# Kernel optimization log

Measured on AMD Instinct MI355X. Metric: run time of the kernel, lower is better.

Reference implementation:

```python
import jax, jax.numpy as jnp
import numpy as np

K = 3          # k_neighbors
EPS = 1e-12    # F.normalize eps


def _l2norm(x):
    n = jnp.sqrt(jnp.sum(x * x, axis=-1, keepdims=True))
    return x / jnp.maximum(n, EPS)


def setup_inputs() -> dict:
    key = jax.random.key(0)
    k1, k2 = jax.random.split(key)
    query_features = jax.random.normal(k1, (64, 64, 32, 32), dtype=jnp.float32)
    support_features = jax.random.normal(k2, (64, 5, 64, 1024), dtype=jnp.float32)
    return {"query_features": query_features, "support_features": support_features}


def reference(query_features, support_features):
    B, D, h, w = query_features.shape
    # (B, Nq, D), L2-normalized along D
    q_local = _l2norm(query_features.reshape(B, D, h * w).transpose(0, 2, 1))
    # support: (B, Way, D, Ns) -> (B, Way, Ns, D), L2-normalized along D
    s_local = _l2norm(support_features.transpose(0, 1, 3, 2))
    # cosine similarities for all (batch, way) pairs in one batched matmul
    sim = jnp.einsum('bqd,bwsd->bwqs', q_local, s_local)  # (B, Way, Nq, Ns)
    k_actual = min(K, sim.shape[-1])
    topk_sim, _ = jax.lax.top_k(sim, k_actual)            # (B, Way, Nq, k)
    return topk_sim.sum(axis=(-1, -2))                    # (B, Way)
```

## Files before the change

### kernel.cpp

```cpp
#include <hip/hip_runtime.h>
#include <hip/hip_bf16.h>


using bf16x8 = __attribute__((ext_vector_type(8))) short;
using f32x4  = __attribute__((ext_vector_type(4))) float;

__device__ inline unsigned short f2bf(float f) {
    unsigned int u = __float_as_uint(f);
    u += 0x7fffu + ((u >> 16) & 1u);
    return (unsigned short)(u >> 16);
}

__device__ inline uint4 pack8(const float* v) {
    uint4 r;
    r.x = (unsigned)f2bf(v[0]) | ((unsigned)f2bf(v[1]) << 16);
    r.y = (unsigned)f2bf(v[2]) | ((unsigned)f2bf(v[3]) << 16);
    r.z = (unsigned)f2bf(v[4]) | ((unsigned)f2bf(v[5]) << 16);
    r.w = (unsigned)f2bf(v[6]) | ((unsigned)f2bf(v[7]) << 16);
    return r;
}

#define INS(v, T0, T1, T2) do {                         \
    float _v = (v);                                     \
    float _n0 = fmaxf((T0), _v);                        \
    float _n1 = __builtin_amdgcn_fmed3f(_v, (T0), (T1));\
    float _n2 = __builtin_amdgcn_fmed3f(_v, (T1), (T2));\
    (T0) = _n0; (T1) = _n1; (T2) = _n2;                 \
} while (0)

__global__ void norms_kernel(const float* __restrict__ Q, const float* __restrict__ S,
                             float* __restrict__ rnq, float* __restrict__ rns) {
    int gid = blockIdx.x * blockDim.x + threadIdx.x;
    if (gid < 65536) {
        int b = gid >> 10, qi = gid & 1023;
        const float* p = Q + (size_t)b * 65536 + qi;
        float ss = 0.f;
        #pragma unroll
        for (int d = 0; d < 64; ++d) { float v = p[(size_t)d * 1024]; ss += v * v; }
        rnq[gid] = 1.0f / fmaxf(sqrtf(ss), 1e-12f);
    } else {
        int v = gid - 65536;
        int bw = v >> 10, si = v & 1023;
        const float* p = S + (size_t)bw * 65536 + si;
        float ss = 0.f;
        #pragma unroll
        for (int d = 0; d < 64; ++d) { float x = p[(size_t)d * 1024]; ss += x * x; }
        rns[v] = 1.0f / fmaxf(sqrtf(ss), 1e-12f);
    }
}

__global__ __launch_bounds__(512) void knn_main(
        const float* __restrict__ Q, const float* __restrict__ S,
        const float* __restrict__ rnq, const float* __restrict__ rns,
        float* __restrict__ partial) {
    __shared__ uint4 qfrag[16 * 128];
    __shared__ uint4 sfrag[2][4 * 128];
    __shared__ float wsum[8];

    const int qc = blockIdx.x, w = blockIdx.y, b = blockIdx.z;
    const int t = threadIdx.x, wv = t >> 6, lane = t & 63;

    const float* Qb   = Q + (size_t)b * 65536;
    const float* Sb   = S + (size_t)(b * 5 + w) * 65536;
    const float* rnqb = rnq + (b << 10);
    const float* rnsb = rns + ((b * 5 + w) << 10);

    for (int sub = 0; sub < 4; ++sub) {
        int qg = (qc << 8) + (sub << 6) + lane;
        float r = rnqb[qg];
        float v[8];
        #pragma unroll
        for (int i = 0; i < 8; ++i)
            v[i] = Qb[(size_t)((wv << 3) + i) * 1024 + qg] * r;
        qfrag[((sub << 2) + (lane >> 4)) * 128 + (wv << 4) + (lane & 15)] = pack8(v);
    }
    __syncthreads();

    bf16x8 bq[2][2];
    #pragma unroll
    for (int qt = 0; qt < 2; ++qt)
        #pragma unroll
        for (int c = 0; c < 2; ++c)
            bq[qt][c] = *reinterpret_cast<const bf16x8*>(
                &qfrag[((wv << 1) + qt) * 128 + (c << 6) + lane]);

    {
        float sv[8]; float rs = rnsb[lane];
        #pragma unroll
        for (int i = 0; i < 8; ++i)
            sv[i] = Sb[(size_t)((wv << 3) + i) * 1024 + lane] * rs;
        sfrag[0][(lane >> 4) * 128 + (wv << 4) + (lane & 15)] = pack8(sv);
    }
    __syncthreads();

    float t0[2] = {-1e30f, -1e30f}, t1[2] = {-1e30f, -1e30f}, t2[2] = {-1e30f, -1e30f};
    int cur = 0;

    for (int blk = 0; blk < 16; ++blk) {
        float sv[8];
        if (blk < 15) {
            const int sb = (blk + 1) << 6;
            float rs = rnsb[sb + lane];
            #pragma unroll
            for (int i = 0; i < 8; ++i)
                sv[i] = Sb[(size_t)((wv << 3) + i) * 1024 + sb + lane] * rs;
        }
        #pragma unroll
        for (int st = 0; st < 4; ++st) {
            bf16x8 a0 = *reinterpret_cast<const bf16x8*>(&sfrag[cur][st * 128 + lane]);
            bf16x8 a1 = *reinterpret_cast<const bf16x8*>(&sfrag[cur][st * 128 + 64 + lane]);
            #pragma unroll
            for (int qt = 0; qt < 2; ++qt) {
                f32x4 c = {0.f, 0.f, 0.f, 0.f};
                c = __builtin_amdgcn_mfma_f32_16x16x32_bf16(a0, bq[qt][0], c, 0, 0, 0);
                c = __builtin_amdgcn_mfma_f32_16x16x32_bf16(a1, bq[qt][1], c, 0, 0, 0);
                #pragma unroll
                for (int j = 0; j < 4; ++j)
                    INS(c[j], t0[qt], t1[qt], t2[qt]);
            }
        }
        if (blk < 15)
            sfrag[cur ^ 1][(lane >> 4) * 128 + (wv << 4) + (lane & 15)] = pack8(sv);
        __syncthreads();
        cur ^= 1;
    }

    #pragma unroll
    for (int qt = 0; qt < 2; ++qt) {
        #pragma unroll
        for (int m = 16; m <= 32; m <<= 1) {
            float b0 = __shfl_xor(t0[qt], m);
            float b1 = __shfl_xor(t1[qt], m);
            float b2 = __shfl_xor(t2[qt], m);
            INS(b0, t0[qt], t1[qt], t2[qt]);
            INS(b1, t0[qt], t1[qt], t2[qt]);
            INS(b2, t0[qt], t1[qt], t2[qt]);
        }
    }
    float s3 = (t0[0] + t1[0] + t2[0]) + (t0[1] + t1[1] + t2[1]);
    #pragma unroll
    for (int m = 1; m < 64; m <<= 1) s3 += __shfl_xor(s3, m);
    s3 *= 0.25f;
    if (lane == 0) wsum[wv] = s3;
    __syncthreads();
    if (t == 0) {
        float acc = 0.f;
        #pragma unroll
        for (int i = 0; i < 8; ++i) acc += wsum[i];
        partial[((size_t)(b * 5 + w) << 2) + qc] = acc;
    }
}

__global__ void finalize_kernel(const float* __restrict__ partial, float* __restrict__ out) {
    int i = blockIdx.x * blockDim.x + threadIdx.x;
    if (i < 320)
        out[i] = (partial[4 * i] + partial[4 * i + 1]) +
                 (partial[4 * i + 2] + partial[4 * i + 3]);
}

extern "C" void kernel_launch(void* const* d_in, const int* in_sizes, int n_in,
                              void* d_out, int out_size, void* d_ws, size_t ws_size,
                              hipStream_t stream) {
    const float* Q = (const float*)d_in[0];
    const float* S = (const float*)d_in[1];
    float* out = (float*)d_out;

    float* rnq = (float*)d_ws;
    float* rns = rnq + 65536;
    float* partial = rns + 327680;

    norms_kernel<<<(65536 + 327680) / 256, 256, 0, stream>>>(Q, S, rnq, rns);
    dim3 grid(4, 5, 64);
    knn_main<<<grid, 512, 0, stream>>>(Q, S, rnq, rns, partial);
    finalize_kernel<<<2, 256, 0, stream>>>(partial, out);
}
```

Before: 108.6 us.

## Double queries per block, defer query normalization, use hardware bf16 pack

Each block now covers 512 queries instead of 256, loading them in two phases through the same shared buffer. Each wave holds four query tiles, so every staged support tile is reused across twice as many MFMAs, and the grid shrinks to half the blocks. Query normalization moves to after top-k: the raw dot products are ranked and the selected sum is scaled by the query's inverse norm, which is valid because that norm is positive and the same for all of a query's candidates. The software bf16 rounding is replaced with the v_cvt_pk_bf16_f32 instruction, and the launch bounds gain an occupancy hint. Risks include higher register pressure from the extra accumulators and fragments, and fewer blocks to fill the GPU.

```diff
diff --git a/kernel.cpp b/kernel.cpp
--- a/kernel.cpp
+++ b/kernel.cpp
@@ -5,18 +5,18 @@
 using bf16x8 = __attribute__((ext_vector_type(8))) short;
 using f32x4  = __attribute__((ext_vector_type(4))) float;
 
-__device__ inline unsigned short f2bf(float f) {
-    unsigned int u = __float_as_uint(f);
-    u += 0x7fffu + ((u >> 16) & 1u);
-    return (unsigned short)(u >> 16);
+__device__ inline unsigned cvt_pk_bf16(float lo, float hi) {
+    unsigned r;
+    asm("v_cvt_pk_bf16_f32 %0, %1, %2" : "=v"(r) : "v"(lo), "v"(hi));
+    return r;
 }
 
-__device__ inline uint4 pack8(const float* v) {
+__device__ inline uint4 pack8cvt(const float* v) {
     uint4 r;
-    r.x = (unsigned)f2bf(v[0]) | ((unsigned)f2bf(v[1]) << 16);
-    r.y = (unsigned)f2bf(v[2]) | ((unsigned)f2bf(v[3]) << 16);
-    r.z = (unsigned)f2bf(v[4]) | ((unsigned)f2bf(v[5]) << 16);
-    r.w = (unsigned)f2bf(v[6]) | ((unsigned)f2bf(v[7]) << 16);
+    r.x = cvt_pk_bf16(v[0], v[1]);
+    r.y = cvt_pk_bf16(v[2], v[3]);
+    r.z = cvt_pk_bf16(v[4], v[5]);
+    r.w = cvt_pk_bf16(v[6], v[7]);
     return r;
 }
 
@@ -49,7 +49,7 @@
     }
 }
 
-__global__ __launch_bounds__(512) void knn_main(
+__global__ __launch_bounds__(512, 4) void knn_main(
         const float* __restrict__ Q, const float* __restrict__ S,
         const float* __restrict__ rnq, const float* __restrict__ rns,
         float* __restrict__ partial) {
@@ -65,52 +65,59 @@
     const float* rnqb = rnq + (b << 10);
     const float* rnsb = rns + ((b * 5 + w) << 10);
 
-    for (int sub = 0; sub < 4; ++sub) {
-        int qg = (qc << 8) + (sub << 6) + lane;
-        float r = rnqb[qg];
-        float v[8];
-        #pragma unroll
-        for (int i = 0; i < 8; ++i)
-            v[i] = Qb[(size_t)((wv << 3) + i) * 1024 + qg] * r;
-        qfrag[((sub << 2) + (lane >> 4)) * 128 + (wv << 4) + (lane & 15)] = pack8(v);
+    bf16x8 bq[4][2];
+    for (int ph = 0; ph < 2; ++ph) {
+        for (int sub = 0; sub < 4; ++sub) {
+            int qg = (qc << 9) + (ph << 8) + (sub << 6) + lane;
+            float v[8];
+            #pragma unroll
+            for (int i = 0; i < 8; ++i)
+                v[i] = Qb[(size_t)((wv << 3) + i) * 1024 + qg];
+            qfrag[((sub << 2) + (lane >> 4)) * 128 + (wv << 4) + (lane & 15)] = pack8cvt(v);
+        }
+        __syncthreads();
+        if ((wv >> 2) == ph) {
+            #pragma unroll
+            for (int qt = 0; qt < 4; ++qt)
+                #pragma unroll
+                for (int c = 0; c < 2; ++c)
+                    bq[qt][c] = *reinterpret_cast<const bf16x8*>(
+                        &qfrag[(((wv & 3) << 2) + qt) * 128 + (c << 6) + lane]);
+        }
+        __syncthreads();
     }
-    __syncthreads();
-
-    bf16x8 bq[2][2];
-    #pragma unroll
-    for (int qt = 0; qt < 2; ++qt)
-        #pragma unroll
-        for (int c = 0; c < 2; ++c)
-            bq[qt][c] = *reinterpret_cast<const bf16x8*>(
-                &qfrag[((wv << 1) + qt) * 128 + (c << 6) + lane]);
 
     {
         float sv[8]; float rs = rnsb[lane];
         #pragma unroll
         for (int i = 0; i < 8; ++i)
             sv[i] = Sb[(size_t)((wv << 3) + i) * 1024 + lane] * rs;
-        sfrag[0][(lane >> 4) * 128 + (wv << 4) + (lane & 15)] = pack8(sv);
+        sfrag[0][(lane >> 4) * 128 + (wv << 4) + (lane & 15)] = pack8cvt(sv);
     }
     __syncthreads();
 
-    float t0[2] = {-1e30f, -1e30f}, t1[2] = {-1e30f, -1e30f}, t2[2] = {-1e30f, -1e30f};
+    float t0[4], t1[4], t2[4];
+    #pragma unroll
+    for (int qt = 0; qt < 4; ++qt) { t0[qt] = -1e30f; t1[qt] = -1e30f; t2[qt] = -1e30f; }
     int cur = 0;
 
+    const float* sp = Sb + ((wv << 3) << 10) + lane;
+
     for (int blk = 0; blk < 16; ++blk) {
-        float sv[8];
+        float sv[8]; float rs;
         if (blk < 15) {
             const int sb = (blk + 1) << 6;
-            float rs = rnsb[sb + lane];
+            rs = rnsb[sb + lane];
             #pragma unroll
             for (int i = 0; i < 8; ++i)
-                sv[i] = Sb[(size_t)((wv << 3) + i) * 1024 + sb + lane] * rs;
+                sv[i] = sp[(size_t)(i << 10) + sb];
         }
         #pragma unroll
         for (int st = 0; st < 4; ++st) {
             bf16x8 a0 = *reinterpret_cast<const bf16x8*>(&sfrag[cur][st * 128 + lane]);
             bf16x8 a1 = *reinterpret_cast<const bf16x8*>(&sfrag[cur][st * 128 + 64 + lane]);
             #pragma unroll
-            for (int qt = 0; qt < 2; ++qt) {
+            for (int qt = 0; qt < 4; ++qt) {
                 f32x4 c = {0.f, 0.f, 0.f, 0.f};
                 c = __builtin_amdgcn_mfma_f32_16x16x32_bf16(a0, bq[qt][0], c, 0, 0, 0);
                 c = __builtin_amdgcn_mfma_f32_16x16x32_bf16(a1, bq[qt][1], c, 0, 0, 0);
@@ -119,14 +126,18 @@
                     INS(c[j], t0[qt], t1[qt], t2[qt]);
             }
         }
-        if (blk < 15)
-            sfrag[cur ^ 1][(lane >> 4) * 128 + (wv << 4) + (lane & 15)] = pack8(sv);
+        if (blk < 15) {
+            #pragma unroll
+            for (int i = 0; i < 8; ++i) sv[i] *= rs;
+            sfrag[cur ^ 1][(lane >> 4) * 128 + (wv << 4) + (lane & 15)] = pack8cvt(sv);
+        }
         __syncthreads();
         cur ^= 1;
     }
 
+    float s3 = 0.f;
     #pragma unroll
-    for (int qt = 0; qt < 2; ++qt) {
+    for (int qt = 0; qt < 4; ++qt) {
         #pragma unroll
         for (int m = 16; m <= 32; m <<= 1) {
             float b0 = __shfl_xor(t0[qt], m);
@@ -136,8 +147,9 @@
             INS(b1, t0[qt], t1[qt], t2[qt]);
             INS(b2, t0[qt], t1[qt], t2[qt]);
         }
+        int qg = (qc << 9) + (wv << 6) + (qt << 4) + (lane & 15);
+        s3 += (t0[qt] + t1[qt] + t2[qt]) * rnqb[qg];
     }
-    float s3 = (t0[0] + t1[0] + t2[0]) + (t0[1] + t1[1] + t2[1]);
     #pragma unroll
     for (int m = 1; m < 64; m <<= 1) s3 += __shfl_xor(s3, m);
     s3 *= 0.25f;
@@ -147,15 +159,14 @@
         float acc = 0.f;
         #pragma unroll
         for (int i = 0; i < 8; ++i) acc += wsum[i];
-        partial[((size_t)(b * 5 + w) << 2) + qc] = acc;
+        partial[((b * 5 + w) << 1) + qc] = acc;
     }
 }
 
 __global__ void finalize_kernel(const float* __restrict__ partial, float* __restrict__ out) {
     int i = blockIdx.x * blockDim.x + threadIdx.x;
     if (i < 320)
-        out[i] = (partial[4 * i] + partial[4 * i + 1]) +
-                 (partial[4 * i + 2] + partial[4 * i + 3]);
+        out[i] = partial[2 * i] + partial[2 * i + 1];
 }
 
 extern "C" void kernel_launch(void* const* d_in, const int* in_sizes, int n_in,
@@ -170,7 +181,7 @@
     float* partial = rns + 327680;
 
     norms_kernel<<<(65536 + 327680) / 256, 256, 0, stream>>>(Q, S, rnq, rns);
-    dim3 grid(4, 5, 64);
+    dim3 grid(2, 5, 64);
     knn_main<<<grid, 512, 0, stream>>>(Q, S, rnq, rns, partial);
     finalize_kernel<<<2, 256, 0, stream>>>(partial, out);
 }
```

New measurement: 100.0 us. 1.09x faster.
